# Kernel optimization log

Hardware: AMD Instinct MI355X
Metric: run time of the kernel (lower is better)

## Reference

```python
import jax, jax.numpy as jnp
import numpy as np

EPS = 1e-7  # Keras binary_crossentropy epsilon


def setup_inputs() -> dict:
    key = jax.random.key(0)
    ks = jax.random.split(key, 4)
    B, D, H = 256, 512, 512
    return {
        "embeddings": jax.random.normal(ks[0], (B, D), dtype=jnp.float32),
        "labels": jax.random.randint(ks[1], (B,), 0, 16),
        "W1": jax.random.normal(ks[2], (2 * D, H), dtype=jnp.float32) / np.float32(np.sqrt(2 * D)),
        "b1": jnp.zeros((H,), jnp.float32),
        "W2": jax.random.normal(ks[3], (H, 1), dtype=jnp.float32) / np.float32(np.sqrt(H)),
        "b2": jnp.zeros((1,), jnp.float32),
    }


def reference(embeddings, labels, W1, b1, W2, b2):
    # All-pairs expansion equivalent to tf.meshgrid + tf.gather over batch indices.
    # Pair (i, j): input1 = embeddings[j] (fast axis), input2 = embeddings[i].
    B, D = embeddings.shape
    x1 = jnp.broadcast_to(embeddings[None, :, :], (B, B, D))
    x2 = jnp.broadcast_to(embeddings[:, None, :], (B, B, D))
    x = jnp.concatenate([x1, x2], axis=-1)  # (B, B, 2D)
    # metric_layer: siamese dense head -> pairwise similarity probability
    h = jax.nn.relu(jnp.einsum('ijd,dh->ijh', x, W1) + b1)          # (B, B, H)
    p = jax.nn.sigmoid(jnp.einsum('ijh,ho->ijo', h, W2) + b2)[..., 0]  # (B, B)
    p = jnp.clip(p, EPS, 1.0 - EPS)
    # target_function: label equality (symmetric, so pair order is irrelevant)
    t = (labels[:, None] == labels[None, :]).astype(p.dtype)        # (B, B)
    # loss: element-wise binary crossentropy over all B^2 pairs
    loss = -(t * jnp.log(p) + (1.0 - t) * jnp.log1p(-p))
    return loss.reshape(-1)  # (B*B,)
```

## Files before the change

kernel.cpp:

```cpp
#include <hip/hip_runtime.h>
#include <math.h>


#define B 256
#define D 512
#define H 512

__global__ __launch_bounds__(256) void head_gemm(
    const float* __restrict__ emb, const float* __restrict__ W1,
    const float* __restrict__ b1, float* __restrict__ A, float* __restrict__ C) {
    __shared__ float sE[8 * D];

    const int z  = blockIdx.z;
    const int r0 = blockIdx.y * 8;
    const int h  = blockIdx.x * 256 + threadIdx.x;

    const float4* src = (const float4*)(emb + (size_t)r0 * D);
    for (int idx = threadIdx.x; idx < (8 * D) / 4; idx += 256)
        ((float4*)sE)[idx] = src[idx];
    __syncthreads();

    float acc[8];
    const float binit = z ? 0.0f : b1[h];
#pragma unroll
    for (int r = 0; r < 8; ++r) acc[r] = binit;

    const float* w = W1 + (size_t)(z * D) * H + h;

#pragma unroll 2
    for (int d = 0; d < D; d += 4) {
        const float w0 = w[(size_t)(d + 0) * H];
        const float w1v = w[(size_t)(d + 1) * H];
        const float w2v = w[(size_t)(d + 2) * H];
        const float w3v = w[(size_t)(d + 3) * H];
#pragma unroll
        for (int r = 0; r < 8; ++r) {
            float4 e = *(const float4*)&sE[r * D + d];
            acc[r] = fmaf(e.x, w0, acc[r]);
            acc[r] = fmaf(e.y, w1v, acc[r]);
            acc[r] = fmaf(e.z, w2v, acc[r]);
            acc[r] = fmaf(e.w, w3v, acc[r]);
        }
    }

    float* dst = z ? C : A;
#pragma unroll
    for (int r = 0; r < 8; ++r) dst[(size_t)(r0 + r) * H + h] = acc[r];
}

#define PADH 516

__global__ __launch_bounds__(256) void pair_loss(
    const float* __restrict__ A, const float* __restrict__ C,
    const float* __restrict__ w2, const float* __restrict__ b2,
    const int* __restrict__ labels, float* __restrict__ out) {
    __shared__ float sA[16][PADH];
    __shared__ float sC[16][PADH];
    __shared__ float sW[H];

    const int j0 = blockIdx.x * 16;
    const int i0 = blockIdx.y * 16;
    const int tid = threadIdx.x;

    for (int idx = tid; idx < 16 * (H / 4); idx += 256) {
        const int r = idx >> 7;
        const int c4 = idx & 127;
        float4 va = ((const float4*)(A + (size_t)(j0 + r) * H))[c4];
        *(float4*)&sA[r][c4 * 4] = va;
        float4 vc = ((const float4*)(C + (size_t)(i0 + r) * H))[c4];
        *(float4*)&sC[r][c4 * 4] = vc;
    }
    for (int idx = tid; idx < H; idx += 256) sW[idx] = w2[idx];
    __syncthreads();

    const int tx = tid & 15;
    const int ty = tid >> 4;

    float s = 0.0f;
#pragma unroll 8
    for (int h = 0; h < H; h += 4) {
        float4 a = *(const float4*)&sA[tx][h];
        float4 c = *(const float4*)&sC[ty][h];
        float4 w = *(const float4*)&sW[h];
        s = fmaf(fmaxf(a.x + c.x, 0.0f), w.x, s);
        s = fmaf(fmaxf(a.y + c.y, 0.0f), w.y, s);
        s = fmaf(fmaxf(a.z + c.z, 0.0f), w.z, s);
        s = fmaf(fmaxf(a.w + c.w, 0.0f), w.w, s);
    }

    const float z = s + b2[0];
    float p = 1.0f / (1.0f + expf(-z));
    p = fminf(fmaxf(p, 1e-7f), 1.0f - 1e-7f);

    const int i = i0 + ty;
    const int j = j0 + tx;
    const float t = (labels[i] == labels[j]) ? 1.0f : 0.0f;
    const float loss = -(t * logf(p) + (1.0f - t) * log1pf(-p));
    out[(size_t)i * B + j] = loss;
}

extern "C" void kernel_launch(void* const* d_in, const int* in_sizes, int n_in,
                              void* d_out, int out_size, void* d_ws, size_t ws_size,
                              hipStream_t stream) {
    const float* emb    = (const float*)d_in[0];
    const int*   labels = (const int*)d_in[1];
    const float* W1     = (const float*)d_in[2];
    const float* b1     = (const float*)d_in[3];
    const float* W2     = (const float*)d_in[4];
    const float* b2     = (const float*)d_in[5];
    float* out = (float*)d_out;

    float* A = (float*)d_ws;
    float* C = A + (size_t)B * H;

    dim3 g1(2, 32, 2);
    head_gemm<<<g1, 256, 0, stream>>>(emb, W1, b1, A, C);

    dim3 g2(16, 16);
    pair_loss<<<g2, 256, 0, stream>>>(A, C, W2, b2, labels, out);
}
```

Measured before the change: 35.80 us.

## Drop LDS staging in head GEMM and compute two pair rows per thread

The head GEMM no longer stages embedding rows in shared memory. It reads them directly from global memory, relying on wave-uniform broadcast loads and the cache, and widens the W1 load batch to 8. The pair-loss kernel halves its block to 128 threads, and each thread accumulates two output rows, reusing the loaded A vector across both. It also reads W2 from global memory instead of LDS. This cuts shared-memory traffic and the sync, at the cost of scalar or global loads and less parallelism per block.

```diff
diff --git a/kernel.cpp b/kernel.cpp
--- a/kernel.cpp
+++ b/kernel.cpp
@@ -9,16 +9,9 @@
 __global__ __launch_bounds__(256) void head_gemm(
     const float* __restrict__ emb, const float* __restrict__ W1,
     const float* __restrict__ b1, float* __restrict__ A, float* __restrict__ C) {
-    __shared__ float sE[8 * D];
-
     const int z  = blockIdx.z;
     const int r0 = blockIdx.y * 8;
     const int h  = blockIdx.x * 256 + threadIdx.x;
-
-    const float4* src = (const float4*)(emb + (size_t)r0 * D);
-    for (int idx = threadIdx.x; idx < (8 * D) / 4; idx += 256)
-        ((float4*)sE)[idx] = src[idx];
-    __syncthreads();
 
     float acc[8];
     const float binit = z ? 0.0f : b1[h];
@@ -26,20 +19,19 @@
     for (int r = 0; r < 8; ++r) acc[r] = binit;
 
     const float* w = W1 + (size_t)(z * D) * H + h;
+    const float* e = emb + (size_t)r0 * D;
 
 #pragma unroll 2
-    for (int d = 0; d < D; d += 4) {
-        const float w0 = w[(size_t)(d + 0) * H];
-        const float w1v = w[(size_t)(d + 1) * H];
-        const float w2v = w[(size_t)(d + 2) * H];
-        const float w3v = w[(size_t)(d + 3) * H];
+    for (int d = 0; d < D; d += 8) {
+        float wv[8];
+#pragma unroll
+        for (int k = 0; k < 8; ++k)
+            wv[k] = w[(size_t)(d + k) * H];
 #pragma unroll
         for (int r = 0; r < 8; ++r) {
-            float4 e = *(const float4*)&sE[r * D + d];
-            acc[r] = fmaf(e.x, w0, acc[r]);
-            acc[r] = fmaf(e.y, w1v, acc[r]);
-            acc[r] = fmaf(e.z, w2v, acc[r]);
-            acc[r] = fmaf(e.w, w3v, acc[r]);
+#pragma unroll
+            for (int k = 0; k < 8; ++k)
+                acc[r] = fmaf(e[r * D + d + k], wv[k], acc[r]);
         }
     }
 
@@ -50,19 +42,18 @@
 
 #define PADH 516
 
-__global__ __launch_bounds__(256) void pair_loss(
+__global__ __launch_bounds__(128) void pair_loss(
     const float* __restrict__ A, const float* __restrict__ C,
     const float* __restrict__ w2, const float* __restrict__ b2,
     const int* __restrict__ labels, float* __restrict__ out) {
     __shared__ float sA[16][PADH];
     __shared__ float sC[16][PADH];
-    __shared__ float sW[H];
 
     const int j0 = blockIdx.x * 16;
     const int i0 = blockIdx.y * 16;
     const int tid = threadIdx.x;
 
-    for (int idx = tid; idx < 16 * (H / 4); idx += 256) {
+    for (int idx = tid; idx < 16 * (H / 4); idx += 128) {
         const int r = idx >> 7;
         const int c4 = idx & 127;
         float4 va = ((const float4*)(A + (size_t)(j0 + r) * H))[c4];
@@ -70,33 +61,42 @@
         float4 vc = ((const float4*)(C + (size_t)(i0 + r) * H))[c4];
         *(float4*)&sC[r][c4 * 4] = vc;
     }
-    for (int idx = tid; idx < H; idx += 256) sW[idx] = w2[idx];
     __syncthreads();
 
     const int tx = tid & 15;
     const int ty = tid >> 4;
 
-    float s = 0.0f;
-#pragma unroll 8
+    float s0 = 0.0f, s1 = 0.0f;
+#pragma unroll 4
     for (int h = 0; h < H; h += 4) {
-        float4 a = *(const float4*)&sA[tx][h];
-        float4 c = *(const float4*)&sC[ty][h];
-        float4 w = *(const float4*)&sW[h];
-        s = fmaf(fmaxf(a.x + c.x, 0.0f), w.x, s);
-        s = fmaf(fmaxf(a.y + c.y, 0.0f), w.y, s);
-        s = fmaf(fmaxf(a.z + c.z, 0.0f), w.z, s);
-        s = fmaf(fmaxf(a.w + c.w, 0.0f), w.w, s);
+        float4 a  = *(const float4*)&sA[tx][h];
+        float4 c0 = *(const float4*)&sC[ty][h];
+        float4 c1 = *(const float4*)&sC[ty + 8][h];
+        float4 w  = *(const float4*)&w2[h];
+        s0 = fmaf(fmaxf(a.x + c0.x, 0.0f), w.x, s0);
+        s0 = fmaf(fmaxf(a.y + c0.y, 0.0f), w.y, s0);
+        s0 = fmaf(fmaxf(a.z + c0.z, 0.0f), w.z, s0);
+        s0 = fmaf(fmaxf(a.w + c0.w, 0.0f), w.w, s0);
+        s1 = fmaf(fmaxf(a.x + c1.x, 0.0f), w.x, s1);
+        s1 = fmaf(fmaxf(a.y + c1.y, 0.0f), w.y, s1);
+        s1 = fmaf(fmaxf(a.z + c1.z, 0.0f), w.z, s1);
+        s1 = fmaf(fmaxf(a.w + c1.w, 0.0f), w.w, s1);
     }
 
-    const float z = s + b2[0];
-    float p = 1.0f / (1.0f + expf(-z));
-    p = fminf(fmaxf(p, 1e-7f), 1.0f - 1e-7f);
+    const float bias = b2[0];
+    const int j = j0 + tx;
+    const int lj = labels[j];
 
-    const int i = i0 + ty;
-    const int j = j0 + tx;
-    const float t = (labels[i] == labels[j]) ? 1.0f : 0.0f;
-    const float loss = -(t * logf(p) + (1.0f - t) * log1pf(-p));
-    out[(size_t)i * B + j] = loss;
+#pragma unroll
+    for (int q = 0; q < 2; ++q) {
+        const int i = i0 + ty + q * 8;
+        const float z = (q ? s1 : s0) + bias;
+        float p = 1.0f / (1.0f + expf(-z));
+        p = fminf(fmaxf(p, 1e-7f), 1.0f - 1e-7f);
+        const float t = (labels[i] == lj) ? 1.0f : 0.0f;
+        const float loss = -(t * logf(p) + (1.0f - t) * log1pf(-p));
+        out[(size_t)i * B + j] = loss;
+    }
 }
 
 extern "C" void kernel_launch(void* const* d_in, const int* in_sizes, int n_in,
@@ -117,5 +117,5 @@
     head_gemm<<<g1, 256, 0, stream>>>(emb, W1, b1, A, C);
 
     dim3 g2(16, 16);
-    pair_loss<<<g2, 256, 0, stream>>>(A, C, W2, b2, labels, out);
+    pair_loss<<<g2, 128, 0, stream>>>(A, C, W2, b2, labels, out);
 }
```

New measurement: 57.80 us. +61.5%, slower.
